# Optimization experiments

Measured on AMD Instinct MI355X. Metric: run time of the kernel, lower is better.

## Reference

```python
import jax, jax.numpy as jnp
import numpy as np

B, Cin, Cout = 2, 32, 16
D, H, W = 48, 64, 128
K = 3
EPS = 1e-5  # BatchNorm3d default eps


def setup_inputs() -> dict:
    key = jax.random.key(0)
    ks = jax.random.split(key, 6)
    return {
        "x": jax.random.normal(ks[0], (B, Cin, D, H, W), jnp.float32),
        "weight": jax.random.normal(ks[1], (Cout, Cin, K, K, K), jnp.float32) * 0.05,
        "gamma": jax.random.uniform(ks[2], (Cout,), jnp.float32, minval=0.5, maxval=1.5),
        "beta": jax.random.normal(ks[3], (Cout,), jnp.float32) * 0.1,
        "running_mean": jax.random.normal(ks[4], (Cout,), jnp.float32) * 0.1,
        "running_var": jax.random.uniform(ks[5], (Cout,), jnp.float32, minval=0.5, maxval=1.5),
    }


def _binarize(v):
    # forward: sign(v) in {-1, 0, +1}; backward (STE): hardtanh grad (pass-through on |v|<=1)
    clipped = jnp.clip(v, -1.0, 1.0)
    return clipped + jax.lax.stop_gradient(jnp.sign(v) - clipped)


def reference(x, weight, gamma, beta, running_mean, running_var):
    b, c, d, h, w = x.shape
    # trilinear upsample, scale (1,2,2), align_corners=False (half-pixel centers)
    x = jax.image.resize(x, (b, c, d, 2 * h, 2 * w), method="trilinear")
    # binarize activations and weights; XNOR-style per-output-channel scale alpha = mean|W|
    xb = _binarize(x)
    alpha = jnp.mean(jnp.abs(weight), axis=(1, 2, 3, 4), keepdims=True)  # [Cout,1,1,1,1]
    wb = _binarize(weight) * alpha
    y = jax.lax.conv_general_dilated(
        xb, wb,
        window_strides=(1, 1, 1),
        padding=[(1, 1), (1, 1), (1, 1)],
        dimension_numbers=("NCDHW", "OIDHW", "NCDHW"),
    )  # [B, Cout, D, 2H, 2W]
    # fused BatchNorm3d (inference form) + ReLU
    inv = gamma / jnp.sqrt(running_var + EPS)
    shift = beta - running_mean * inv
    y = y * inv[None, :, None, None, None] + shift[None, :, None, None, None]
    return jax.nn.relu(y)
```

## Files before the change

kernel.cpp:

```cpp
#include <hip/hip_runtime.h>
#include <hip/hip_bf16.h>
#include <stdint.h>

#define BB   2
#define CIN  32
#define COUT 16
#define DD   48
#define HIN  64
#define WIN  128
#define H2   128
#define W2   256
#define PLANE_WORDS (H2 * W2)

__global__ __launch_bounds__(512) void ibc3d_prep(
    const float* __restrict__ wgt, const float* __restrict__ gamma,
    const float* __restrict__ beta, const float* __restrict__ rmean,
    const float* __restrict__ rvar, uint32_t* __restrict__ bw,
    float* __restrict__ scale, float* __restrict__ shift)
{
    int t = threadIdx.x;
    if (t < 27 * 16) {
        int tap = t >> 4, co = t & 15;
        uint32_t word = 0;
        for (int ci = 0; ci < CIN; ++ci) {
            float v = wgt[(co * CIN + ci) * 27 + tap];
            word |= (v > 0.0f ? 1u : 0u) << ci;
        }
        bw[t] = word;
    } else if (t < 27 * 16 + 16) {
        int co = t - 27 * 16;
        double s = 0.0;
        for (int i = 0; i < CIN * 27; ++i)
            s += fabs((double)wgt[co * CIN * 27 + i]);
        float alpha = (float)(s / (double)(CIN * 27));
        float inv = gamma[co] / sqrtf(rvar[co] + 1e-5f);
        scale[co] = alpha * inv;
        shift[co] = beta[co] - rmean[co] * inv;
    }
}

__device__ __forceinline__ uint32_t pack_word(const float* __restrict__ x,
                                              int b, int d, int h2, int w2)
{
    int m = h2 >> 1, dh = h2 & 1;
    int n = w2 >> 1, dwp = w2 & 1;
    int rA = m + dh - 1;
    int rB = rA + 1;
    double wA = dh ? 0.75 : 0.25;
    double wB = 1.0 - wA;
    rA = rA < 0 ? 0 : rA;
    rB = rB > (HIN - 1) ? (HIN - 1) : rB;
    int cA = n + dwp - 1;
    int cB = cA + 1;
    double wC = dwp ? 0.75 : 0.25;
    double wD = 1.0 - wC;
    cA = cA < 0 ? 0 : cA;
    cB = cB > (WIN - 1) ? (WIN - 1) : cB;

    const float* xp = x + ((size_t)b * CIN * DD + d) * (HIN * WIN);
    int oA = rA * WIN, oB = rB * WIN;
    uint32_t word = 0;
    for (int ci = 0; ci < CIN; ++ci) {
        const float* xc = xp + (size_t)ci * (DD * HIN * WIN);
        float a0 = xc[oA + cA], a1 = xc[oA + cB];
        float b0 = xc[oB + cA], b1 = xc[oB + cB];
        double t0 = wA * (double)a0 + wB * (double)b0;
        double t1 = wA * (double)a1 + wB * (double)b1;
        double v  = wC * t0 + wD * t1;
        word |= (v >= 0.0 ? 1u : 0u) << ci;
    }
    return word;
}

__global__ __launch_bounds__(256) void ibc3d_packq(
    const float* __restrict__ x, uint32_t* __restrict__ bx,
    int b_start, int nplanes)
{
    int idx = blockIdx.x * 256 + threadIdx.x;
    int n  = idx & (WIN - 1);
    int m  = (idx >> 7) & (HIN - 1);
    int pl = idx >> 13;
    if (pl >= nplanes) return;
    int d  = pl % DD;
    int b  = b_start + pl / DD;

    int rm1 = m > 0 ? m - 1 : 0;
    int rp1 = m < HIN - 1 ? m + 1 : HIN - 1;
    int cm1 = n > 0 ? n - 1 : 0;
    int cp1 = n < WIN - 1 ? n + 1 : WIN - 1;

    const float* xp = x + ((size_t)b * CIN * DD + d) * (HIN * WIN);
    int o0 = rm1 * WIN, o1 = m * WIN, o2 = rp1 * WIN;

    uint32_t w00 = 0, w01 = 0, w10 = 0, w11 = 0;
#pragma unroll 4
    for (int ci = 0; ci < CIN; ++ci) {
        const float* xc = xp + (size_t)ci * (DD * HIN * WIN);
        float a00 = xc[o0 + cm1], a01 = xc[o0 + n], a02 = xc[o0 + cp1];
        float a10 = xc[o1 + cm1], a11 = xc[o1 + n], a12 = xc[o1 + cp1];
        float a20 = xc[o2 + cm1], a21 = xc[o2 + n], a22 = xc[o2 + cp1];

        float u0r0 = 0.25f * a00 + 0.75f * a01, u1r0 = 0.75f * a01 + 0.25f * a02;
        float u0r1 = 0.25f * a10 + 0.75f * a11, u1r1 = 0.75f * a11 + 0.25f * a12;
        float u0r2 = 0.25f * a20 + 0.75f * a21, u1r2 = 0.75f * a21 + 0.25f * a22;

        float v00 = 0.25f * u0r0 + 0.75f * u0r1;
        float v01 = 0.25f * u1r0 + 0.75f * u1r1;
        float v10 = 0.75f * u0r1 + 0.25f * u0r2;
        float v11 = 0.75f * u1r1 + 0.25f * u1r2;

        uint32_t s00, s01, s10, s11;
        float amin = fminf(fminf(fabsf(v00), fabsf(v01)),
                           fminf(fabsf(v10), fabsf(v11)));
        if (__builtin_expect(amin < 1e-5f, 0)) {
            double d00 = a00, d01 = a01, d02 = a02;
            double d10 = a10, d11 = a11, d12 = a12;
            double d20 = a20, d21 = a21, d22 = a22;
            double e0r0 = 0.25 * d00 + 0.75 * d01, e1r0 = 0.75 * d01 + 0.25 * d02;
            double e0r1 = 0.25 * d10 + 0.75 * d11, e1r1 = 0.75 * d11 + 0.25 * d12;
            double e0r2 = 0.25 * d20 + 0.75 * d21, e1r2 = 0.75 * d21 + 0.25 * d22;
            s00 = (0.25 * e0r0 + 0.75 * e0r1) >= 0.0;
            s01 = (0.25 * e1r0 + 0.75 * e1r1) >= 0.0;
            s10 = (0.75 * e0r1 + 0.25 * e0r2) >= 0.0;
            s11 = (0.75 * e1r1 + 0.25 * e1r2) >= 0.0;
        } else {
            s00 = v00 >= 0.0f;
            s01 = v01 >= 0.0f;
            s10 = v10 >= 0.0f;
            s11 = v11 >= 0.0f;
        }
        w00 |= s00 << ci; w01 |= s01 << ci;
        w10 |= s10 << ci; w11 |= s11 << ci;
    }

    size_t base = (size_t)pl * PLANE_WORDS + (size_t)(2 * m) * W2 + 2 * n;
    *(uint2*)(bx + base)      = make_uint2(w00, w01);
    *(uint2*)(bx + base + W2) = make_uint2(w10, w11);
}

__global__ __launch_bounds__(256) void ibc3d_conv3(
    const uint32_t* __restrict__ bx, const uint32_t* __restrict__ bwg,
    const float* __restrict__ scaleg, const float* __restrict__ shiftg,
    float* __restrict__ out, int b_start)
{
    int bid   = blockIdx.x;
    int h2    = bid & (H2 - 1);
    int plane = bid >> 7;
    int d     = plane % DD;
    int b     = b_start + plane / DD;
    int w2    = threadIdx.x;

    int acc[16];
#pragma unroll
    for (int c = 0; c < 16; ++c) acc[c] = 0;

#pragma unroll
    for (int kd = 0; kd < 3; ++kd) {
        int dd = d + kd - 1;
        if (dd < 0 || dd >= DD) continue;
        const uint32_t* bxp = bx + (size_t)(plane + kd - 1) * PLANE_WORDS;
#pragma unroll
        for (int kh = 0; kh < 3; ++kh) {
            int hh = h2 + kh - 1;
            if (hh < 0 || hh >= H2) continue;
            const uint32_t* brow = bxp + hh * W2;
#pragma unroll
            for (int kw = 0; kw < 3; ++kw) {
                int ww = w2 + kw - 1;
                if (ww >= 0 && ww < W2) {
                    uint32_t word = brow[ww];
                    int tap = kd * 9 + kh * 3 + kw;
#pragma unroll
                    for (int co = 0; co < 16; ++co)
                        acc[co] += __popc(word ^ bwg[tap * 16 + co]);
                }
            }
        }
    }

    int nd = 1 + (d > 0)  + (d < DD - 1);
    int nh = 1 + (h2 > 0) + (h2 < H2 - 1);
    int nw = 1 + (w2 > 0) + (w2 < W2 - 1);
    float base = 32.0f * (float)(nd * nh * nw);

    size_t obase = (((size_t)(b * COUT) * DD + d) * H2 + h2) * W2 + w2;
#pragma unroll
    for (int co = 0; co < 16; ++co) {
        float y = (base - 2.0f * (float)acc[co]) * scaleg[co] + shiftg[co];
        y = y > 0.0f ? y : 0.0f;
        out[obase + (size_t)co * (DD * H2 * W2)] = y;
    }
}

__global__ __launch_bounds__(256) void ibc3d_fused(
    const float* __restrict__ x, const float* __restrict__ wgt,
    const float* __restrict__ gamma, const float* __restrict__ beta,
    const float* __restrict__ rmean, const float* __restrict__ rvar,
    float* __restrict__ out)
{
    __shared__ uint32_t sbw[27 * 16];
    __shared__ float sscale[16];
    __shared__ float sshift[16];
    __shared__ uint32_t sw[3][10][264];

    int tid = threadIdx.x;
    for (int t = tid; t < 27 * 16; t += 256) {
        int tap = t >> 4, co = t & 15;
        uint32_t word = 0;
        for (int ci = 0; ci < CIN; ++ci) {
            float v = wgt[(co * CIN + ci) * 27 + tap];
            word |= (v > 0.0f ? 1u : 0u) << ci;
        }
        sbw[t] = word;
    }
    if (tid < 16) {
        int co = tid;
        double s = 0.0;
        for (int i = 0; i < CIN * 27; ++i)
            s += fabs((double)wgt[co * CIN * 27 + i]);
        float alpha = (float)(s / (double)(CIN * 27));
        float inv = gamma[co] / sqrtf(rvar[co] + 1e-5f);
        sscale[co] = alpha * inv;
        sshift[co] = beta[co] - rmean[co] * inv;
    }

    int bid = blockIdx.x;
    int hq  = bid & 15;
    int r   = bid >> 4;
    int b   = r / DD;
    int d   = r % DD;
    int h2base = hq * 8;

    for (int i = tid; i < 3 * 10 * 258; i += 256) {
        int kd  = i / 2580;
        int rem = i - kd * 2580;
        int ri  = rem / 258;
        int ciw = rem - ri * 258;
        int dd = d + kd - 1;
        int h2 = h2base - 1 + ri;
        int w2 = ciw - 1;
        uint32_t word = 0;
        if (dd >= 0 && dd < DD && h2 >= 0 && h2 < H2 && w2 >= 0 && w2 < W2)
            word = pack_word(x, b, dd, h2, w2);
        sw[kd][ri][ciw] = word;
    }
    __syncthreads();

    int w2 = tid;
    for (int p = 0; p < 8; ++p) {
        int h2 = h2base + p;
        int acc[16];
#pragma unroll
        for (int c = 0; c < 16; ++c) acc[c] = 0;
        int nv = 0;
        for (int kd = 0; kd < 3; ++kd) {
            int dd = d + kd - 1;
            if (dd < 0 || dd >= DD) continue;
            for (int kh = 0; kh < 3; ++kh) {
                int hh = h2 + kh - 1;
                if (hh < 0 || hh >= H2) continue;
                for (int kw = 0; kw < 3; ++kw) {
                    int ww = w2 + kw - 1;
                    if (ww < 0 || ww >= W2) continue;
                    uint32_t word = sw[kd][p + kh][w2 + kw];
                    nv += 1;
                    int tap = kd * 9 + kh * 3 + kw;
#pragma unroll
                    for (int co = 0; co < 16; ++co)
                        acc[co] += __popc(word ^ sbw[tap * 16 + co]);
                }
            }
        }
        float base = 32.0f * (float)nv;
#pragma unroll
        for (int co = 0; co < 16; ++co) {
            float y = (base - 2.0f * (float)acc[co]) * sscale[co] + sshift[co];
            y = y > 0.0f ? y : 0.0f;
            size_t oidx = (((size_t)(b * COUT + co) * DD + d) * H2 + h2) * W2 + w2;
            out[oidx] = y;
        }
    }
}

extern "C" void kernel_launch(void* const* d_in, const int* in_sizes, int n_in,
                              void* d_out, int out_size, void* d_ws, size_t ws_size,
                              hipStream_t stream)
{
    (void)in_sizes; (void)n_in; (void)out_size;
    const float* x     = (const float*)d_in[0];
    const float* wgt   = (const float*)d_in[1];
    const float* gamma = (const float*)d_in[2];
    const float* beta  = (const float*)d_in[3];
    const float* rmean = (const float*)d_in[4];
    const float* rvar  = (const float*)d_in[5];
    float* out = (float*)d_out;

    const size_t HDR = 4096;
    const size_t bx_full = (size_t)BB * DD * PLANE_WORDS * 4;
    const size_t bx_half = (size_t)DD * PLANE_WORDS * 4;

    if (d_ws != nullptr && ws_size >= HDR + bx_full) {
        uint8_t* ws = (uint8_t*)d_ws;
        uint32_t* bw    = (uint32_t*)ws;
        float*    scale = (float*)(ws + 2048);
        float*    shift = (float*)(ws + 2112);
        uint32_t* bx    = (uint32_t*)(ws + HDR);
        ibc3d_prep<<<1, 512, 0, stream>>>(wgt, gamma, beta, rmean, rvar, bw, scale, shift);
        int nplanes = BB * DD;
        ibc3d_packq<<<nplanes * 32, 256, 0, stream>>>(x, bx, 0, nplanes);
        ibc3d_conv3<<<nplanes * H2, 256, 0, stream>>>(bx, bw, scale, shift, out, 0);
    } else if (d_ws != nullptr && ws_size >= HDR + bx_half) {
        uint8_t* ws = (uint8_t*)d_ws;
        uint32_t* bw    = (uint32_t*)ws;
        float*    scale = (float*)(ws + 2048);
        float*    shift = (float*)(ws + 2112);
        uint32_t* bx    = (uint32_t*)(ws + HDR);
        ibc3d_prep<<<1, 512, 0, stream>>>(wgt, gamma, beta, rmean, rvar, bw, scale, shift);
        for (int b = 0; b < BB; ++b) {
            ibc3d_packq<<<DD * 32, 256, 0, stream>>>(x, bx, b, DD);
            ibc3d_conv3<<<DD * H2, 256, 0, stream>>>(bx, bw, scale, shift, out, b);
        }
    } else {
        ibc3d_fused<<<BB * DD * (H2 / 8), 256, 0, stream>>>(
            x, wgt, gamma, beta, rmean, rvar, out);
    }
}
```

Measured before the change: 162.1 us.

## Register-block conv over four output rows and widen pack to two input columns

The binary conv kernel now computes four consecutive output rows per thread. Each loaded row word is reused across up to three row accumulators, so global loads drop from 9 to 6 rows per 4 outputs. The block index is remapped in an XCD-style interleave. The pack kernel now handles two input columns per thread, reusing the neighbour loads and writing uint4. The cost is higher register pressure (64 int accumulators), which may reduce occupancy, and fewer blocks.

New measurement: 201.3 us (median of 4 runs). 24.2% more time.

```diff
diff --git a/kernel.cpp b/kernel.cpp
--- a/kernel.cpp
+++ b/kernel.cpp
@@ -72,87 +72,104 @@
     return word;
 }
 
-__global__ __launch_bounds__(256) void ibc3d_packq(
+__global__ __launch_bounds__(256) void ibc3d_packq2(
     const float* __restrict__ x, uint32_t* __restrict__ bx,
     int b_start, int nplanes)
 {
     int idx = blockIdx.x * 256 + threadIdx.x;
-    int n  = idx & (WIN - 1);
-    int m  = (idx >> 7) & (HIN - 1);
-    int pl = idx >> 13;
+    int j  = idx & 63;
+    int m  = (idx >> 6) & 63;
+    int pl = idx >> 12;
     if (pl >= nplanes) return;
     int d  = pl % DD;
     int b  = b_start + pl / DD;
 
     int rm1 = m > 0 ? m - 1 : 0;
     int rp1 = m < HIN - 1 ? m + 1 : HIN - 1;
-    int cm1 = n > 0 ? n - 1 : 0;
-    int cp1 = n < WIN - 1 ? n + 1 : WIN - 1;
+    int c0  = 2 * j;
+    int cm1 = c0 > 0 ? c0 - 1 : 0;
+    int c1  = c0 + 1;
+    int cp2 = c0 + 2 < WIN - 1 ? c0 + 2 : WIN - 1;
 
     const float* xp = x + ((size_t)b * CIN * DD + d) * (HIN * WIN);
     int o0 = rm1 * WIN, o1 = m * WIN, o2 = rp1 * WIN;
 
-    uint32_t w00 = 0, w01 = 0, w10 = 0, w11 = 0;
+    uint32_t w0[4] = {0, 0, 0, 0};
+    uint32_t w1[4] = {0, 0, 0, 0};
 #pragma unroll 4
     for (int ci = 0; ci < CIN; ++ci) {
         const float* xc = xp + (size_t)ci * (DD * HIN * WIN);
-        float a00 = xc[o0 + cm1], a01 = xc[o0 + n], a02 = xc[o0 + cp1];
-        float a10 = xc[o1 + cm1], a11 = xc[o1 + n], a12 = xc[o1 + cp1];
-        float a20 = xc[o2 + cm1], a21 = xc[o2 + n], a22 = xc[o2 + cp1];
-
-        float u0r0 = 0.25f * a00 + 0.75f * a01, u1r0 = 0.75f * a01 + 0.25f * a02;
-        float u0r1 = 0.25f * a10 + 0.75f * a11, u1r1 = 0.75f * a11 + 0.25f * a12;
-        float u0r2 = 0.25f * a20 + 0.75f * a21, u1r2 = 0.75f * a21 + 0.25f * a22;
+        float a0m = xc[o0 + cm1], a00 = xc[o0 + c0], a01 = xc[o0 + c1], a0p = xc[o0 + cp2];
+        float a1m = xc[o1 + cm1], a10 = xc[o1 + c0], a11 = xc[o1 + c1], a1p = xc[o1 + cp2];
+        float a2m = xc[o2 + cm1], a20 = xc[o2 + c0], a21 = xc[o2 + c1], a2p = xc[o2 + cp2];
+
+        float u0r0 = 0.25f * a0m + 0.75f * a00, u1r0 = 0.75f * a00 + 0.25f * a01;
+        float u2r0 = 0.25f * a00 + 0.75f * a01, u3r0 = 0.75f * a01 + 0.25f * a0p;
+        float u0r1 = 0.25f * a1m + 0.75f * a10, u1r1 = 0.75f * a10 + 0.25f * a11;
+        float u2r1 = 0.25f * a10 + 0.75f * a11, u3r1 = 0.75f * a11 + 0.25f * a1p;
+        float u0r2 = 0.25f * a2m + 0.75f * a20, u1r2 = 0.75f * a20 + 0.25f * a21;
+        float u2r2 = 0.25f * a20 + 0.75f * a21, u3r2 = 0.75f * a21 + 0.25f * a2p;
 
         float v00 = 0.25f * u0r0 + 0.75f * u0r1;
         float v01 = 0.25f * u1r0 + 0.75f * u1r1;
+        float v02 = 0.25f * u2r0 + 0.75f * u2r1;
+        float v03 = 0.25f * u3r0 + 0.75f * u3r1;
         float v10 = 0.75f * u0r1 + 0.25f * u0r2;
         float v11 = 0.75f * u1r1 + 0.25f * u1r2;
-
-        uint32_t s00, s01, s10, s11;
-        float amin = fminf(fminf(fabsf(v00), fabsf(v01)),
-                           fminf(fabsf(v10), fabsf(v11)));
+        float v12 = 0.75f * u2r1 + 0.25f * u2r2;
+        float v13 = 0.75f * u3r1 + 0.25f * u3r2;
+
+        uint32_t s00, s01, s02, s03, s10, s11, s12, s13;
+        float amin = fminf(fminf(fminf(fabsf(v00), fabsf(v01)), fminf(fabsf(v02), fabsf(v03))),
+                           fminf(fminf(fabsf(v10), fabsf(v11)), fminf(fabsf(v12), fabsf(v13))));
         if (__builtin_expect(amin < 1e-5f, 0)) {
-            double d00 = a00, d01 = a01, d02 = a02;
-            double d10 = a10, d11 = a11, d12 = a12;
-            double d20 = a20, d21 = a21, d22 = a22;
-            double e0r0 = 0.25 * d00 + 0.75 * d01, e1r0 = 0.75 * d01 + 0.25 * d02;
-            double e0r1 = 0.25 * d10 + 0.75 * d11, e1r1 = 0.75 * d11 + 0.25 * d12;
-            double e0r2 = 0.25 * d20 + 0.75 * d21, e1r2 = 0.75 * d21 + 0.25 * d22;
+            double e0r0 = 0.25 * (double)a0m + 0.75 * (double)a00, e1r0 = 0.75 * (double)a00 + 0.25 * (double)a01;
+            double e2r0 = 0.25 * (double)a00 + 0.75 * (double)a01, e3r0 = 0.75 * (double)a01 + 0.25 * (double)a0p;
+            double e0r1 = 0.25 * (double)a1m + 0.75 * (double)a10, e1r1 = 0.75 * (double)a10 + 0.25 * (double)a11;
+            double e2r1 = 0.25 * (double)a10 + 0.75 * (double)a11, e3r1 = 0.75 * (double)a11 + 0.25 * (double)a1p;
+            double e0r2 = 0.25 * (double)a2m + 0.75 * (double)a20, e1r2 = 0.75 * (double)a20 + 0.25 * (double)a21;
+            double e2r2 = 0.25 * (double)a20 + 0.75 * (double)a21, e3r2 = 0.75 * (double)a21 + 0.25 * (double)a2p;
             s00 = (0.25 * e0r0 + 0.75 * e0r1) >= 0.0;
             s01 = (0.25 * e1r0 + 0.75 * e1r1) >= 0.0;
+            s02 = (0.25 * e2r0 + 0.75 * e2r1) >= 0.0;
+            s03 = (0.25 * e3r0 + 0.75 * e3r1) >= 0.0;
             s10 = (0.75 * e0r1 + 0.25 * e0r2) >= 0.0;
             s11 = (0.75 * e1r1 + 0.25 * e1r2) >= 0.0;
+            s12 = (0.75 * e2r1 + 0.25 * e2r2) >= 0.0;
+            s13 = (0.75 * e3r1 + 0.25 * e3r2) >= 0.0;
         } else {
-            s00 = v00 >= 0.0f;
-            s01 = v01 >= 0.0f;
-            s10 = v10 >= 0.0f;
-            s11 = v11 >= 0.0f;
-        }
-        w00 |= s00 << ci; w01 |= s01 << ci;
-        w10 |= s10 << ci; w11 |= s11 << ci;
-    }
-
-    size_t base = (size_t)pl * PLANE_WORDS + (size_t)(2 * m) * W2 + 2 * n;
-    *(uint2*)(bx + base)      = make_uint2(w00, w01);
-    *(uint2*)(bx + base + W2) = make_uint2(w10, w11);
-}
-
-__global__ __launch_bounds__(256) void ibc3d_conv3(
+            s00 = v00 >= 0.0f; s01 = v01 >= 0.0f; s02 = v02 >= 0.0f; s03 = v03 >= 0.0f;
+            s10 = v10 >= 0.0f; s11 = v11 >= 0.0f; s12 = v12 >= 0.0f; s13 = v13 >= 0.0f;
+        }
+        w0[0] |= s00 << ci; w0[1] |= s01 << ci; w0[2] |= s02 << ci; w0[3] |= s03 << ci;
+        w1[0] |= s10 << ci; w1[1] |= s11 << ci; w1[2] |= s12 << ci; w1[3] |= s13 << ci;
+    }
+
+    size_t base = (size_t)pl * PLANE_WORDS + (size_t)(2 * m) * W2 + 4 * j;
+    *(uint4*)(bx + base)      = make_uint4(w0[0], w0[1], w0[2], w0[3]);
+    *(uint4*)(bx + base + W2) = make_uint4(w1[0], w1[1], w1[2], w1[3]);
+}
+
+__global__ __launch_bounds__(256) void ibc3d_conv4(
     const uint32_t* __restrict__ bx, const uint32_t* __restrict__ bwg,
     const float* __restrict__ scaleg, const float* __restrict__ shiftg,
     float* __restrict__ out, int b_start)
 {
-    int bid   = blockIdx.x;
-    int h2    = bid & (H2 - 1);
-    int plane = bid >> 7;
+    int per = gridDim.x >> 3;
+    int bid = (blockIdx.x & 7) * per + (blockIdx.x >> 3);
+
+    int hq    = bid & 31;
+    int plane = bid >> 5;
     int d     = plane % DD;
     int b     = b_start + plane / DD;
     int w2    = threadIdx.x;
-
-    int acc[16];
-#pragma unroll
-    for (int c = 0; c < 16; ++c) acc[c] = 0;
+    int h2b   = hq * 4;
+
+    int acc[4][16];
+#pragma unroll
+    for (int p = 0; p < 4; ++p)
+#pragma unroll
+        for (int c = 0; c < 16; ++c) acc[p][c] = 0;
 
 #pragma unroll
     for (int kd = 0; kd < 3; ++kd) {
@@ -160,8 +177,8 @@
         if (dd < 0 || dd >= DD) continue;
         const uint32_t* bxp = bx + (size_t)(plane + kd - 1) * PLANE_WORDS;
 #pragma unroll
-        for (int kh = 0; kh < 3; ++kh) {
-            int hh = h2 + kh - 1;
+        for (int r = 0; r < 6; ++r) {
+            int hh = h2b - 1 + r;
             if (hh < 0 || hh >= H2) continue;
             const uint32_t* brow = bxp + hh * W2;
 #pragma unroll
@@ -169,26 +186,35 @@
                 int ww = w2 + kw - 1;
                 if (ww >= 0 && ww < W2) {
                     uint32_t word = brow[ww];
-                    int tap = kd * 9 + kh * 3 + kw;
-#pragma unroll
-                    for (int co = 0; co < 16; ++co)
-                        acc[co] += __popc(word ^ bwg[tap * 16 + co]);
+#pragma unroll
+                    for (int p = 0; p < 4; ++p) {
+                        if (p > r || p + 2 < r) continue;
+                        int kh = r - p;
+                        int tap = kd * 9 + kh * 3 + kw;
+#pragma unroll
+                        for (int co = 0; co < 16; ++co)
+                            acc[p][co] += __popc(word ^ bwg[tap * 16 + co]);
+                    }
                 }
             }
         }
     }
 
-    int nd = 1 + (d > 0)  + (d < DD - 1);
-    int nh = 1 + (h2 > 0) + (h2 < H2 - 1);
+    int nd = 1 + (d > 0) + (d < DD - 1);
     int nw = 1 + (w2 > 0) + (w2 < W2 - 1);
-    float base = 32.0f * (float)(nd * nh * nw);
-
-    size_t obase = (((size_t)(b * COUT) * DD + d) * H2 + h2) * W2 + w2;
-#pragma unroll
-    for (int co = 0; co < 16; ++co) {
-        float y = (base - 2.0f * (float)acc[co]) * scaleg[co] + shiftg[co];
-        y = y > 0.0f ? y : 0.0f;
-        out[obase + (size_t)co * (DD * H2 * W2)] = y;
+
+    size_t obase = (((size_t)(b * COUT) * DD + d) * H2 + h2b) * W2 + w2;
+#pragma unroll
+    for (int p = 0; p < 4; ++p) {
+        int h2 = h2b + p;
+        int nh = 1 + (h2 > 0) + (h2 < H2 - 1);
+        float base = 32.0f * (float)(nd * nh * nw);
+#pragma unroll
+        for (int co = 0; co < 16; ++co) {
+            float y = (base - 2.0f * (float)acc[p][co]) * scaleg[co] + shiftg[co];
+            y = y > 0.0f ? y : 0.0f;
+            out[obase + (size_t)co * (DD * H2 * W2) + (size_t)p * W2] = y;
+        }
     }
 }
 
@@ -307,8 +333,8 @@
         uint32_t* bx    = (uint32_t*)(ws + HDR);
         ibc3d_prep<<<1, 512, 0, stream>>>(wgt, gamma, beta, rmean, rvar, bw, scale, shift);
         int nplanes = BB * DD;
-        ibc3d_packq<<<nplanes * 32, 256, 0, stream>>>(x, bx, 0, nplanes);
-        ibc3d_conv3<<<nplanes * H2, 256, 0, stream>>>(bx, bw, scale, shift, out, 0);
+        ibc3d_packq2<<<nplanes * 16, 256, 0, stream>>>(x, bx, 0, nplanes);
+        ibc3d_conv4<<<nplanes * 32, 256, 0, stream>>>(bx, bw, scale, shift, out, 0);
     } else if (d_ws != nullptr && ws_size >= HDR + bx_half) {
         uint8_t* ws = (uint8_t*)d_ws;
         uint32_t* bw    = (uint32_t*)ws;
@@ -317,8 +343,8 @@
         uint32_t* bx    = (uint32_t*)(ws + HDR);
         ibc3d_prep<<<1, 512, 0, stream>>>(wgt, gamma, beta, rmean, rvar, bw, scale, shift);
         for (int b = 0; b < BB; ++b) {
-            ibc3d_packq<<<DD * 32, 256, 0, stream>>>(x, bx, b, DD);
-            ibc3d_conv3<<<DD * H2, 256, 0, stream>>>(bx, bw, scale, shift, out, b);
+            ibc3d_packq2<<<DD * 16, 256, 0, stream>>>(x, bx, b, DD);
+            ibc3d_conv4<<<DD * 32, 256, 0, stream>>>(bx, bw, scale, shift, out, b);
         }
     } else {
         ibc3d_fused<<<BB * DD * (H2 / 8), 256, 0, stream>>>(
```
